# Kernel tuning notes

Measured on AMD Instinct MI355X. Metric: run time of the kernel, lower is better.

The kernel has to match this reference:

```python
import jax, jax.numpy as jnp
import numpy as np

B, C, P, T, H = 4, 256, 1024, 64, 8
D = C // H
SCALE = float(np.sqrt(D * T))


def setup_inputs() -> dict:
    key = jax.random.key(0)
    ks = jax.random.split(key, 7)
    s = 1.0 / np.sqrt(C)
    return {
        "x": jax.random.normal(ks[0], (B, C, P, T), dtype=jnp.float32),
        "Wk": jax.random.uniform(ks[1], (C, C), dtype=jnp.float32, minval=-s, maxval=s),
        "bk": jax.random.uniform(ks[2], (C,), dtype=jnp.float32, minval=-s, maxval=s),
        "Wq": jax.random.uniform(ks[3], (C, C), dtype=jnp.float32, minval=-s, maxval=s),
        "bq": jax.random.uniform(ks[4], (C,), dtype=jnp.float32, minval=-s, maxval=s),
        "Wv": jax.random.uniform(ks[5], (C, C), dtype=jnp.float32, minval=-s, maxval=s),
        "bv": jax.random.uniform(ks[6], (C,), dtype=jnp.float32, minval=-s, maxval=s),
    }


def _proj_split(x, W, b):
    # 1x1 conv == channel-mixing linear; then split heads: b (h d) p t -> b h d p t
    y = jnp.einsum('bcpt,oc->bopt', x, W) + b[None, :, None, None]
    Bs, _, Ps, Ts = y.shape
    return y.reshape(Bs, H, D, Ps, Ts)


def reference(x, Wk, bk, Wq, bq, Wv, bv):
    k = _proj_split(x, Wk, bk)
    q = _proj_split(x, Wq, bq)
    v = _proj_split(x, Wv, bv)
    # contract jointly over d and t
    energy = jnp.einsum('bhdpt,bhdqt->bhpq', k, q)
    attn = jax.nn.softmax(energy / SCALE, axis=-1)
    out = jnp.einsum('bhpq,bhdpt->bhdqt', attn, v)
    # merge heads: b h d q t -> b (h d) q t
    return out.reshape(B, C, P, T)
```

## Files before the change

### kernel.cpp

```cpp
#include <hip/hip_runtime.h>
#include <cstdint>
#include <cstddef>

#define NB 4
#define NC 256
#define NP 1024
#define NT 64
#define NH 8
#define ND 32
#define NF 2048
#define NPT 65536
#define KQV_ELEMS 67108864ull
#define INV_SCALE 0.022097086912079608f

typedef unsigned short u16;
typedef __bf16 bf16x8 __attribute__((ext_vector_type(8)));
typedef short  s16x8  __attribute__((ext_vector_type(8)));
typedef short  s16x4  __attribute__((ext_vector_type(4)));
typedef float  f32x4  __attribute__((ext_vector_type(4)));

__device__ __forceinline__ u16 f2bf(float f) {
  unsigned u = __builtin_bit_cast(unsigned, f);
  u += 0x7fffu + ((u >> 16) & 1u);
  return (u16)(u >> 16);
}
__device__ __forceinline__ float bf2f(u16 h) {
  unsigned u = ((unsigned)h) << 16;
  return __builtin_bit_cast(float, u);
}
__device__ __forceinline__ int swz(int row) { return ((row ^ (row >> 3)) & 7) << 4; }

#define GLOAD_LDS16(gp, lp) __builtin_amdgcn_global_load_lds( \
    (const __attribute__((address_space(1))) void*)(gp),      \
    (__attribute__((address_space(3))) void*)(lp), 16, 0, 0)

__device__ __forceinline__ f32x4 mfma16(bf16x8 a, bf16x8 b, f32x4 c) {
  return __builtin_amdgcn_mfma_f32_16x16x32_bf16(a, b, c, 0, 0, 0);
}

__global__ __launch_bounds__(256) void wcast_kernel(
    const float* __restrict__ Wk, const float* __restrict__ Wq,
    const float* __restrict__ Wv, u16* __restrict__ wbf)
{
  int pj = blockIdx.y;
  const float* W = (pj == 0) ? Wk : ((pj == 1) ? Wq : Wv);
  int idx = blockIdx.x * 1024 + threadIdx.x * 4;
  float4 v = *(const float4*)(W + idx);
  s16x4 pk;
  pk[0] = (short)f2bf(v.x); pk[1] = (short)f2bf(v.y);
  pk[2] = (short)f2bf(v.z); pk[3] = (short)f2bf(v.w);
  *(s16x4*)(wbf + (size_t)pj * 65536 + idx) = pk;
}

__global__ __launch_bounds__(256, 2) void xcast_kernel(
    const float* __restrict__ x, u16* __restrict__ xT)
{
  int ptt = blockIdx.x;
  int ct  = blockIdx.y;
  int b   = blockIdx.z;
  __shared__ __align__(16) u16 L[64 * 64];
  int tid = threadIdx.x;
#pragma unroll
  for (int i = 0; i < 4; i++) {
    int cl  = i * 16 + (tid >> 4);
    int ptl = (tid & 15) * 4;
    float4 v = *(const float4*)(x + ((size_t)(b * NC + ct * 64 + cl)) * NPT +
                                ptt * 64 + ptl);
    s16x4 pk;
    pk[0] = (short)f2bf(v.x); pk[1] = (short)f2bf(v.y);
    pk[2] = (short)f2bf(v.z); pk[3] = (short)f2bf(v.w);
    *(s16x4*)((char*)L + ((cl * 128 + ptl * 2) ^ swz(cl))) = pk;
  }
  __syncthreads();
#pragma unroll
  for (int i = 0; i < 2; i++) {
    int ptl = i * 32 + (tid >> 3);
    int c8  = (tid & 7) * 8;
    s16x8 v;
#pragma unroll
    for (int j = 0; j < 8; j++) {
      int row = c8 + j;
      v[j] = (short)*(const u16*)((char*)L + ((row * 128 + ptl * 2) ^ swz(row)));
    }
    *(s16x8*)(xT + ((size_t)b * NPT + (size_t)ptt * 64 + ptl) * NC + ct * 64 + c8) = v;
  }
}

template <int KT>
__device__ __forceinline__ void gemm_core(const u16* __restrict__ A,
                                          const u16* __restrict__ Bp,
                                          u16* As, u16* Bs, f32x4 acc[4][4])
{
  const int tid = threadIdx.x, lane = tid & 63, wave = tid >> 6;
  const int wm = (wave >> 1) * 64, wn = (wave & 1) * 64;
  for (int ks = 0; ks < KT / 64; ks++) {
    const int k0 = ks * 64;
    __syncthreads();
#pragma unroll
    for (int i = 0; i < 4; i++) {
      int r0 = wave * 32 + i * 8;
      int row = r0 + (lane >> 3);
      int col = k0 + (lane & 7) * 8;
      GLOAD_LDS16(A  + (size_t)row * KT + col, &As[r0 * 64]);
      GLOAD_LDS16(Bp + (size_t)row * KT + col, &Bs[r0 * 64]);
    }
    __syncthreads();
#pragma unroll
    for (int kk = 0; kk < 2; kk++) {
      bf16x8 af[4], bfr[4];
#pragma unroll
      for (int f = 0; f < 4; f++) {
        int ra = wm + f * 16 + (lane & 15);
        af[f]  = *(const bf16x8*)((char*)As + ra * 128 + kk * 64 + (lane >> 4) * 16);
        int rb = wn + f * 16 + (lane & 15);
        bfr[f] = *(const bf16x8*)((char*)Bs + rb * 128 + kk * 64 + (lane >> 4) * 16);
      }
#pragma unroll
      for (int fm = 0; fm < 4; fm++)
#pragma unroll
        for (int fn = 0; fn < 4; fn++)
          acc[fm][fn] = mfma16(af[fm], bfr[fn], acc[fm][fn]);
    }
  }
}

__global__ __launch_bounds__(256, 2) void proj_kernel(
    const u16* __restrict__ wbf, const u16* __restrict__ xT,
    const float* __restrict__ bk, const float* __restrict__ bq,
    const float* __restrict__ bv, u16* __restrict__ kqv)
{
  int d0 = blockIdx.x;
  int b  = blockIdx.y;
  int xcd = d0 & 7, r = d0 >> 3;
  int j = r % 6, tch = r / 6;
  int ptile = tch * 8 + xcd;
  int pj = j >> 1, mt = j & 1;
  const float* bias = (pj == 0) ? bk : ((pj == 1) ? bq : bv);
  u16* outb = kqv + (size_t)pj * KQV_ELEMS;

  const int m0 = mt * 128;
  const int n0 = ptile * 128;

  const u16* A  = wbf + (size_t)pj * 65536 + (size_t)m0 * NC;
  const u16* Bp = xT + ((size_t)b * NPT + (size_t)n0) * NC;

  __shared__ __align__(16) u16 SB[2][128 * 64];

  f32x4 acc[4][4];
#pragma unroll
  for (int a = 0; a < 4; a++)
#pragma unroll
    for (int c = 0; c < 4; c++) acc[a][c] = (f32x4){0.f, 0.f, 0.f, 0.f};

  gemm_core<NC>(A, Bp, SB[0], SB[1], acc);

  const int tid  = threadIdx.x;
  const int lane = tid & 63, wave = tid >> 6;
  const int wm = (wave >> 1) * 64, wn = (wave & 1) * 64;

  __syncthreads();
  u16* Lt = &SB[0][0];
#pragma unroll
  for (int fm = 0; fm < 4; fm++) {
#pragma unroll
    for (int jj = 0; jj < 4; jj++) {
      int m = wm + fm * 16 + (lane >> 4) * 4 + jj;
      float bsv = bias[m0 + m];
#pragma unroll
      for (int fn = 0; fn < 4; fn++) {
        int n = wn + fn * 16 + (lane & 15);
        Lt[m * 128 + n] = f2bf(acc[fm][fn][jj] + bsv);
      }
    }
  }
  __syncthreads();

  const int p0 = ptile * 2;
#pragma unroll
  for (int i = 0; i < 8; i++) {
    int hh = mt * 4 + (i >> 1);
    int p  = p0 + (i & 1);
    s16x8 v = *(const s16x8*)(Lt + ((i >> 1) * 32 + (tid >> 3)) * 128 +
                              (i & 1) * 64 + (tid & 7) * 8);
    *(s16x8*)(outb + ((size_t)(b * NH + hh) * NP + p) * NF + tid * 8) = v;
  }
}

__global__ __launch_bounds__(256, 2) void transpose_kernel(
    const u16* __restrict__ in, u16* __restrict__ outp)
{
  int ft = blockIdx.x;
  int pt = blockIdx.y;
  int slab = blockIdx.z;
  __shared__ __align__(16) u16 L[64 * 64];
  int t = threadIdx.x;
  const u16* ip = in + (size_t)slab * NP * NF;
#pragma unroll
  for (int i = 0; i < 2; i++) {
    int pl = i * 32 + (t >> 3);
    int c8 = (t & 7) * 8;
    s16x8 v = *(const s16x8*)(ip + (size_t)(pt * 64 + pl) * NF + ft * 64 + c8);
    *(s16x8*)((char*)L + ((pl * 128 + c8 * 2) ^ swz(pl))) = v;
  }
  __syncthreads();
  u16* op = outp + (size_t)slab * NP * NF;
#pragma unroll
  for (int i = 0; i < 2; i++) {
    int fl = i * 32 + (t >> 3);
    int p8 = (t & 7) * 8;
    s16x8 v;
#pragma unroll
    for (int j2 = 0; j2 < 8; j2++) {
      int row = p8 + j2;
      v[j2] = (short)*(const u16*)((char*)L + ((row * 128 + fl * 2) ^ swz(row)));
    }
    *(s16x8*)(op + (size_t)(ft * 64 + fl) * NP + pt * 64 + p8) = v;
  }
}

#define STG1(TT, I, OP) do {                                                   \
    const u16* gp_ = (OP ? Bg : Ag) + (size_t)grow[I] * KT + (TT) * 32 + gcol[I]; \
    GLOAD_LDS16(gp_, L + ((((TT) & 3) * 32768 + (OP) * 16384 +                 \
                           ((I) & 1 ? W1 : W0)) >> 1));                        \
  } while (0)

#define FENCE() do {                                                           \
    asm volatile("" ::: "memory");                                             \
    __builtin_amdgcn_sched_barrier(0);                                         \
  } while (0)

#define KBODY(J, WAITASM, DOSTG) do {                                          \
    const int bufb_ = ((J) & 3) * 32768;                                       \
    bf16x8 a_[4], b_[4];                                                       \
    _Pragma("unroll")                                                          \
    for (int mf = 0; mf < 4; mf++)                                             \
      a_[mf] = *(const bf16x8*)((const char*)L + bufb_ + baseA + mf * 1024);   \
    _Pragma("unroll")                                                          \
    for (int nf = 0; nf < 4; nf++)                                             \
      b_[nf] = *(const bf16x8*)((const char*)L + bufb_ + baseB + nf * 1024);   \
    if (DOSTG) { STG1((J) + 3, 0, 0); STG1((J) + 3, 1, 0); }                   \
    __builtin_amdgcn_s_barrier();                                              \
    asm volatile("s_waitcnt lgkmcnt(0)" ::: "memory");                         \
    __builtin_amdgcn_sched_barrier(0);                                         \
    __builtin_amdgcn_s_setprio(1);                                             \
    _Pragma("unroll")                                                          \
    for (int mf = 0; mf < 4; mf++)                                             \
      _Pragma("unroll")                                                        \
      for (int nf = 0; nf < 4; nf++)                                           \
        acc[mf][nf] = mfma16(a_[mf], b_[nf], acc[mf][nf]);                     \
    __builtin_amdgcn_s_setprio(0);                                             \
    __builtin_amdgcn_sched_barrier(0);                                         \
    __builtin_amdgcn_s_barrier();                                              \
    FENCE();                                                                   \
    bf16x8 a2_[4];                                                             \
    _Pragma("unroll")                                                          \
    for (int mf = 0; mf < 4; mf++)                                             \
      a2_[mf] = *(const bf16x8*)((const char*)L + bufb_ + baseA +              \
                                 (4 + mf) * 1024);                             \
    if (DOSTG) { STG1((J) + 3, 2, 1); STG1((J) + 3, 3, 1); }                   \
    __builtin_amdgcn_s_barrier();                                              \
    asm volatile("s_waitcnt lgkmcnt(0)" ::: "memory");                         \
    __builtin_amdgcn_sched_barrier(0);                                         \
    __builtin_amdgcn_s_setprio(1);                                             \
    _Pragma("unroll")                                                          \
    for (int mf = 0; mf < 4; mf++)                                             \
      _Pragma("unroll")                                                        \
      for (int nf = 0; nf < 4; nf++)                                           \
        acc[4 + mf][nf] = mfma16(a2_[mf], b_[nf], acc[4 + mf][nf]);            \
    __builtin_amdgcn_s_setprio(0);                                             \
    __builtin_amdgcn_sched_barrier(0);                                         \
    asm volatile(WAITASM ::: "memory");                                        \
    __builtin_amdgcn_s_barrier();                                              \
    FENCE();                                                                   \
  } while (0)

template <int KT>
__device__ __forceinline__ void core256(const u16* __restrict__ Ag,
                                        const u16* __restrict__ Bg,
                                        u16* L, f32x4 acc[8][4])
{
  constexpr int NKT = KT / 32;
  const int tid  = threadIdx.x;
  const int lane = tid & 63;
  const int wv   = tid >> 6;
  const int wr = wv >> 2, wc = wv & 3;

  int grow[4], gcol[4];
#pragma unroll
  for (int i = 0; i < 4; i++) {
    int oi   = (tid + (i & 1) * 512) * 16;
    int loff = oi ^ (((oi >> 6) & 3) << 4);
    grow[i] = loff >> 6;
    gcol[i] = (loff & 63) >> 1;
  }
  const int W0 = wv * 1024;
  const int W1 = wv * 1024 + 8192;

  const int rowA  = wr * 128 + (lane & 15);
  const int baseA = rowA * 64 + (((lane >> 4) * 16) ^ ((rowA & 3) << 4));
  const int rowB  = wc * 64 + (lane & 15);
  const int baseB = 16384 + rowB * 64 + (((lane >> 4) * 16) ^ ((rowB & 3) << 4));

#pragma unroll
  for (int tt = 0; tt < 3; tt++) {
    STG1(tt, 0, 0); STG1(tt, 1, 0); STG1(tt, 2, 1); STG1(tt, 3, 1);
  }
  __builtin_amdgcn_sched_barrier(0);
  asm volatile("s_waitcnt vmcnt(8)" ::: "memory");
  __builtin_amdgcn_s_barrier();
  FENCE();

  for (int j = 0; j < NKT - 3; ++j)
    KBODY(j, "s_waitcnt vmcnt(8)", 1);
  KBODY(NKT - 3, "s_waitcnt vmcnt(4)", 0);
  KBODY(NKT - 2, "s_waitcnt vmcnt(0)", 0);
  KBODY(NKT - 1, "", 0);
}

__global__ __launch_bounds__(512, 2) void qk256_kernel(
    const u16* __restrict__ kb, const u16* __restrict__ qb, u16* __restrict__ S)
{
  extern __shared__ u16 L[];
  int bid = blockIdx.x;
  int xcd = bid & 7, r = bid >> 3;
  int bh  = xcd * 4 + (r >> 4);
  int til = r & 15;
  int mt  = til >> 2, nt = til & 3;

  const u16* Ag = qb + (size_t)bh * NP * NF + (size_t)mt * 256 * NF;
  const u16* Bg = kb + (size_t)bh * NP * NF + (size_t)nt * 256 * NF;

  f32x4 acc[8][4];
#pragma unroll
  for (int a = 0; a < 8; a++)
#pragma unroll
    for (int c = 0; c < 4; c++) acc[a][c] = (f32x4){0.f, 0.f, 0.f, 0.f};

  core256<NF>(Ag, Bg, L, acc);

  const int lane = threadIdx.x & 63, wv = threadIdx.x >> 6;
  const int wr = wv >> 2, wc = wv & 3;
  u16* Sp = S + (size_t)bh * NP * NP;
#pragma unroll
  for (int mf = 0; mf < 8; mf++)
#pragma unroll
    for (int jj = 0; jj < 4; jj++) {
      int m = mt * 256 + wr * 128 + mf * 16 + (lane >> 4) * 4 + jj;
#pragma unroll
      for (int nf = 0; nf < 4; nf++) {
        int n = nt * 256 + wc * 64 + nf * 16 + (lane & 15);
        Sp[(size_t)m * NP + n] = f2bf(acc[mf][nf][jj] * INV_SCALE);
      }
    }
}

__global__ __launch_bounds__(512, 2) void av256_kernel(
    const u16* __restrict__ Ab, const u16* __restrict__ Vt, float* __restrict__ out)
{
  extern __shared__ u16 L[];
  int bid = blockIdx.x;
  int xcd = bid & 7, r = bid >> 3;
  int bh  = xcd * 4 + (r >> 5);
  int til = r & 31;
  int mt  = til >> 3, ntf = til & 7;

  const u16* Ag = Ab + (size_t)bh * NP * NP + (size_t)mt * 256 * NP;
  const u16* Bg = Vt + (size_t)bh * NF * NP + (size_t)ntf * 256 * NP;

  f32x4 acc[8][4];
#pragma unroll
  for (int a = 0; a < 8; a++)
#pragma unroll
    for (int c = 0; c < 4; c++) acc[a][c] = (f32x4){0.f, 0.f, 0.f, 0.f};

  core256<NP>(Ag, Bg, L, acc);

  const int lane = threadIdx.x & 63, wv = threadIdx.x >> 6;
  const int wr = wv >> 2, wc = wv & 3;
  int b = bh >> 3, h = bh & 7;
#pragma unroll
  for (int mf = 0; mf < 8; mf++)
#pragma unroll
    for (int jj = 0; jj < 4; jj++) {
      int m = mt * 256 + wr * 128 + mf * 16 + (lane >> 4) * 4 + jj;
#pragma unroll
      for (int nf = 0; nf < 4; nf++) {
        int n = ntf * 256 + wc * 64 + nf * 16 + (lane & 15);
        int dd = n >> 6, t = n & 63;
        out[((size_t)(b * NC + h * ND + dd) * NP + m) * NT + t] = acc[mf][nf][jj];
      }
    }
}

__global__ __launch_bounds__(256, 2) void softmax_kernel(
    const u16* __restrict__ S, u16* __restrict__ A)
{
  int cb = blockIdx.x;
  int bh = blockIdx.y;
  int tid = threadIdx.x;
  int cg  = tid & 31;
  int qs  = tid >> 5;
  int col0 = cb * 256 + cg * 8;
  const u16* Sp = S + (size_t)bh * NP * NP + col0;

  float m[8], l[8];
#pragma unroll
  for (int j2 = 0; j2 < 8; j2++) { m[j2] = -1e30f; l[j2] = 0.f; }
  for (int q = qs * 128; q < qs * 128 + 128; q++) {
    s16x8 v = *(const s16x8*)(Sp + (size_t)q * NP);
#pragma unroll
    for (int j2 = 0; j2 < 8; j2++) {
      float f = bf2f((u16)v[j2]);
      float mn = fmaxf(m[j2], f);
      l[j2] = l[j2] * __expf(m[j2] - mn) + __expf(f - mn);
      m[j2] = mn;
    }
  }
  __shared__ float ms[8][256], ls[8][256];
#pragma unroll
  for (int j2 = 0; j2 < 8; j2++) {
    ms[qs][cg * 8 + j2] = m[j2];
    ls[qs][cg * 8 + j2] = l[j2];
  }
  __syncthreads();
  float M[8], Li[8];
#pragma unroll
  for (int j2 = 0; j2 < 8; j2++) {
    int c = cg * 8 + j2;
    float mm = ms[0][c];
#pragma unroll
    for (int k = 1; k < 8; k++) mm = fmaxf(mm, ms[k][c]);
    float ll = 0.f;
#pragma unroll
    for (int k = 0; k < 8; k++) ll += ls[k][c] * __expf(ms[k][c] - mm);
    M[j2] = mm; Li[j2] = 1.f / ll;
  }
  u16* Ap = A + (size_t)bh * NP * NP + col0;
  for (int q = qs * 128; q < qs * 128 + 128; q++) {
    s16x8 v = *(const s16x8*)(Sp + (size_t)q * NP);
    s16x8 o;
#pragma unroll
    for (int j2 = 0; j2 < 8; j2++)
      o[j2] = (short)f2bf(__expf(bf2f((u16)v[j2]) - M[j2]) * Li[j2]);
    *(s16x8*)(Ap + (size_t)q * NP) = o;
  }
}

extern "C" void kernel_launch(void* const* d_in, const int* in_sizes, int n_in,
                              void* d_out, int out_size, void* d_ws, size_t ws_size,
                              hipStream_t stream)
{
  if (ws_size < 4ull * KQV_ELEMS * sizeof(u16)) return;

  const float* x  = (const float*)d_in[0];
  const float* Wk = (const float*)d_in[1];
  const float* bk = (const float*)d_in[2];
  const float* Wq = (const float*)d_in[3];
  const float* bq = (const float*)d_in[4];
  const float* Wv = (const float*)d_in[5];
  const float* bv = (const float*)d_in[6];

  u16* kb = (u16*)d_ws;
  u16* qb = kb + KQV_ELEMS;
  u16* vb = kb + 2 * KQV_ELEMS;
  u16* vt = kb + 3 * KQV_ELEMS;

  u16* xT  = (u16*)d_out;
  u16* wbf = xT + KQV_ELEMS;
  u16* Sb  = xT + KQV_ELEMS + 262144;
  u16* Ab  = kb;

  (void)hipFuncSetAttribute((const void*)qk256_kernel,
                            hipFuncAttributeMaxDynamicSharedMemorySize, 131072);
  (void)hipFuncSetAttribute((const void*)av256_kernel,
                            hipFuncAttributeMaxDynamicSharedMemorySize, 131072);

  wcast_kernel<<<dim3(64, 3), 256, 0, stream>>>(Wk, Wq, Wv, wbf);
  xcast_kernel<<<dim3(1024, 4, 4), 256, 0, stream>>>(x, xT);
  proj_kernel<<<dim3(3072, 4), 256, 0, stream>>>(wbf, xT, bk, bq, bv, kb);
  transpose_kernel<<<dim3(32, 16, 32), 256, 0, stream>>>(vb, vt);
  qk256_kernel<<<dim3(512), 512, 131072, stream>>>(kb, qb, Sb);
  softmax_kernel<<<dim3(4, 32), 256, 0, stream>>>(Sb, Ab);
  av256_kernel<<<dim3(1024), 512, 131072, stream>>>(Ab, vt, (float*)d_out);
}
```

Before: 773.6 us.

## Use 256x256 core for projection GEMM and widen softmax grid

```diff
diff --git a/kernel.cpp b/kernel.cpp
--- a/kernel.cpp
+++ b/kernel.cpp
@@ -83,106 +83,6 @@
       v[j] = (short)*(const u16*)((char*)L + ((row * 128 + ptl * 2) ^ swz(row)));
     }
     *(s16x8*)(xT + ((size_t)b * NPT + (size_t)ptt * 64 + ptl) * NC + ct * 64 + c8) = v;
-  }
-}
-
-template <int KT>
-__device__ __forceinline__ void gemm_core(const u16* __restrict__ A,
-                                          const u16* __restrict__ Bp,
-                                          u16* As, u16* Bs, f32x4 acc[4][4])
-{
-  const int tid = threadIdx.x, lane = tid & 63, wave = tid >> 6;
-  const int wm = (wave >> 1) * 64, wn = (wave & 1) * 64;
-  for (int ks = 0; ks < KT / 64; ks++) {
-    const int k0 = ks * 64;
-    __syncthreads();
-#pragma unroll
-    for (int i = 0; i < 4; i++) {
-      int r0 = wave * 32 + i * 8;
-      int row = r0 + (lane >> 3);
-      int col = k0 + (lane & 7) * 8;
-      GLOAD_LDS16(A  + (size_t)row * KT + col, &As[r0 * 64]);
-      GLOAD_LDS16(Bp + (size_t)row * KT + col, &Bs[r0 * 64]);
-    }
-    __syncthreads();
-#pragma unroll
-    for (int kk = 0; kk < 2; kk++) {
-      bf16x8 af[4], bfr[4];
-#pragma unroll
-      for (int f = 0; f < 4; f++) {
-        int ra = wm + f * 16 + (lane & 15);
-        af[f]  = *(const bf16x8*)((char*)As + ra * 128 + kk * 64 + (lane >> 4) * 16);
-        int rb = wn + f * 16 + (lane & 15);
-        bfr[f] = *(const bf16x8*)((char*)Bs + rb * 128 + kk * 64 + (lane >> 4) * 16);
-      }
-#pragma unroll
-      for (int fm = 0; fm < 4; fm++)
-#pragma unroll
-        for (int fn = 0; fn < 4; fn++)
-          acc[fm][fn] = mfma16(af[fm], bfr[fn], acc[fm][fn]);
-    }
-  }
-}
-
-__global__ __launch_bounds__(256, 2) void proj_kernel(
-    const u16* __restrict__ wbf, const u16* __restrict__ xT,
-    const float* __restrict__ bk, const float* __restrict__ bq,
-    const float* __restrict__ bv, u16* __restrict__ kqv)
-{
-  int d0 = blockIdx.x;
-  int b  = blockIdx.y;
-  int xcd = d0 & 7, r = d0 >> 3;
-  int j = r % 6, tch = r / 6;
-  int ptile = tch * 8 + xcd;
-  int pj = j >> 1, mt = j & 1;
-  const float* bias = (pj == 0) ? bk : ((pj == 1) ? bq : bv);
-  u16* outb = kqv + (size_t)pj * KQV_ELEMS;
-
-  const int m0 = mt * 128;
-  const int n0 = ptile * 128;
-
-  const u16* A  = wbf + (size_t)pj * 65536 + (size_t)m0 * NC;
-  const u16* Bp = xT + ((size_t)b * NPT + (size_t)n0) * NC;
-
-  __shared__ __align__(16) u16 SB[2][128 * 64];
-
-  f32x4 acc[4][4];
-#pragma unroll
-  for (int a = 0; a < 4; a++)
-#pragma unroll
-    for (int c = 0; c < 4; c++) acc[a][c] = (f32x4){0.f, 0.f, 0.f, 0.f};
-
-  gemm_core<NC>(A, Bp, SB[0], SB[1], acc);
-
-  const int tid  = threadIdx.x;
-  const int lane = tid & 63, wave = tid >> 6;
-  const int wm = (wave >> 1) * 64, wn = (wave & 1) * 64;
-
-  __syncthreads();
-  u16* Lt = &SB[0][0];
-#pragma unroll
-  for (int fm = 0; fm < 4; fm++) {
-#pragma unroll
-    for (int jj = 0; jj < 4; jj++) {
-      int m = wm + fm * 16 + (lane >> 4) * 4 + jj;
-      float bsv = bias[m0 + m];
-#pragma unroll
-      for (int fn = 0; fn < 4; fn++) {
-        int n = wn + fn * 16 + (lane & 15);
-        Lt[m * 128 + n] = f2bf(acc[fm][fn][jj] + bsv);
-      }
-    }
-  }
-  __syncthreads();
-
-  const int p0 = ptile * 2;
-#pragma unroll
-  for (int i = 0; i < 8; i++) {
-    int hh = mt * 4 + (i >> 1);
-    int p  = p0 + (i & 1);
-    s16x8 v = *(const s16x8*)(Lt + ((i >> 1) * 32 + (tid >> 3)) * 128 +
-                              (i & 1) * 64 + (tid & 7) * 8);
-    *(s16x8*)(outb + ((size_t)(b * NH + hh) * NP + p) * NF + tid * 8) = v;
   }
 }
 
@@ -317,6 +217,52 @@
   KBODY(NKT - 1, "", 0);
 }
 
+__global__ __launch_bounds__(512, 1) void proj256_kernel(
+    const u16* __restrict__ wbf, const u16* __restrict__ xT,
+    const float* __restrict__ bk, const float* __restrict__ bq,
+    const float* __restrict__ bv, u16* __restrict__ kqv)
+{
+  extern __shared__ u16 L[];
+  int d0 = blockIdx.x;
+  int b  = blockIdx.y;
+  int xcd = d0 & 7, r = d0 >> 3;
+  int pj  = r % 3, tch = r / 3;
+  int ptile = tch * 8 + xcd;
+  const float* bias = (pj == 0) ? bk : ((pj == 1) ? bq : bv);
+  u16* outb = kqv + (size_t)pj * KQV_ELEMS;
+  const int n0 = ptile * 256;
+
+  const u16* Ag = wbf + (size_t)pj * 65536;
+  const u16* Bg = xT + ((size_t)b * NPT + (size_t)n0) * NC;
+
+  f32x4 acc[8][4];
+#pragma unroll
+  for (int a = 0; a < 8; a++)
+#pragma unroll
+    for (int c = 0; c < 4; c++) acc[a][c] = (f32x4){0.f, 0.f, 0.f, 0.f};
+
+  core256<NC>(Ag, Bg, L, acc);
+
+  const int lane = threadIdx.x & 63, wv = threadIdx.x >> 6;
+  const int wr = wv >> 2, wc = wv & 3;
+#pragma unroll
+  for (int mf = 0; mf < 8; mf++) {
+#pragma unroll
+    for (int jj = 0; jj < 4; jj++) {
+      int o = wr * 128 + mf * 16 + (lane >> 4) * 4 + jj;
+      float bsv = bias[o];
+      int hh = o >> 5, dd = o & 31;
+#pragma unroll
+      for (int nf = 0; nf < 4; nf++) {
+        int n = n0 + wc * 64 + nf * 16 + (lane & 15);
+        int p = n >> 6, t = n & 63;
+        outb[((size_t)(b * NH + hh) * NP + p) * NF + dd * 64 + t] =
+            f2bf(acc[mf][nf][jj] + bsv);
+      }
+    }
+  }
+}
+
 __global__ __launch_bounds__(512, 2) void qk256_kernel(
     const u16* __restrict__ kb, const u16* __restrict__ qb, u16* __restrict__ S)
 {
@@ -398,15 +344,15 @@
   int cb = blockIdx.x;
   int bh = blockIdx.y;
   int tid = threadIdx.x;
-  int cg  = tid & 31;
-  int qs  = tid >> 5;
-  int col0 = cb * 256 + cg * 8;
+  int cg  = tid & 7;
+  int qs  = tid >> 3;
+  int col0 = cb * 64 + cg * 8;
   const u16* Sp = S + (size_t)bh * NP * NP + col0;
 
   float m[8], l[8];
 #pragma unroll
   for (int j2 = 0; j2 < 8; j2++) { m[j2] = -1e30f; l[j2] = 0.f; }
-  for (int q = qs * 128; q < qs * 128 + 128; q++) {
+  for (int q = qs * 32; q < qs * 32 + 32; q++) {
     s16x8 v = *(const s16x8*)(Sp + (size_t)q * NP);
 #pragma unroll
     for (int j2 = 0; j2 < 8; j2++) {
@@ -416,7 +362,7 @@
       m[j2] = mn;
     }
   }
-  __shared__ float ms[8][256], ls[8][256];
+  __shared__ float ms[32][64], ls[32][64];
 #pragma unroll
   for (int j2 = 0; j2 < 8; j2++) {
     ms[qs][cg * 8 + j2] = m[j2];
@@ -429,14 +375,14 @@
     int c = cg * 8 + j2;
     float mm = ms[0][c];
 #pragma unroll
-    for (int k = 1; k < 8; k++) mm = fmaxf(mm, ms[k][c]);
+    for (int k = 1; k < 32; k++) mm = fmaxf(mm, ms[k][c]);
     float ll = 0.f;
 #pragma unroll
-    for (int k = 0; k < 8; k++) ll += ls[k][c] * __expf(ms[k][c] - mm);
+    for (int k = 0; k < 32; k++) ll += ls[k][c] * __expf(ms[k][c] - mm);
     M[j2] = mm; Li[j2] = 1.f / ll;
   }
   u16* Ap = A + (size_t)bh * NP * NP + col0;
-  for (int q = qs * 128; q < qs * 128 + 128; q++) {
+  for (int q = qs * 32; q < qs * 32 + 32; q++) {
     s16x8 v = *(const s16x8*)(Sp + (size_t)q * NP);
     s16x8 o;
 #pragma unroll
@@ -470,6 +416,8 @@
   u16* Sb  = xT + KQV_ELEMS + 262144;
   u16* Ab  = kb;
 
+  (void)hipFuncSetAttribute((const void*)proj256_kernel,
+                            hipFuncAttributeMaxDynamicSharedMemorySize, 131072);
   (void)hipFuncSetAttribute((const void*)qk256_kernel,
                             hipFuncAttributeMaxDynamicSharedMemorySize, 131072);
   (void)hipFuncSetAttribute((const void*)av256_kernel,
@@ -477,9 +425,9 @@
 
   wcast_kernel<<<dim3(64, 3), 256, 0, stream>>>(Wk, Wq, Wv, wbf);
   xcast_kernel<<<dim3(1024, 4, 4), 256, 0, stream>>>(x, xT);
-  proj_kernel<<<dim3(3072, 4), 256, 0, stream>>>(wbf, xT, bk, bq, bv, kb);
+  proj256_kernel<<<dim3(768, 4), 512, 131072, stream>>>(wbf, xT, bk, bq, bv, kb);
   transpose_kernel<<<dim3(32, 16, 32), 256, 0, stream>>>(vb, vt);
   qk256_kernel<<<dim3(512), 512, 131072, stream>>>(kb, qb, Sb);
-  softmax_kernel<<<dim3(4, 32), 256, 0, stream>>>(Sb, Ab);
+  softmax_kernel<<<dim3(16, 32), 256, 0, stream>>>(Sb, Ab);
   av256_kernel<<<dim3(1024), 512, 131072, stream>>>(Ab, vt, (float*)d_out);
 }
```

After: 672.9 us. -13.0%, faster.
